# Kernel optimization log

Measured on AMD Instinct MI355X. Metric: run time of the kernel, lower is better.

## Reference

```python
import jax, jax.numpy as jnp
import numpy as np

IN_F = 4096
OUT_F = 11008
GROUP = 128
BATCH = 32
Q_OUT = OUT_F // 2          # two int4 values packed per byte along out dim
N_GROUPS = IN_F // GROUP    # 32 groups


def setup_inputs() -> dict:
    key = jax.random.key(0)
    k1, k2, k3, k4, k5 = jax.random.split(key, 5)
    inp = jax.random.normal(k1, (BATCH, 1, IN_F), dtype=jnp.float32)
    qweight = jax.random.randint(k2, (IN_F, Q_OUT), 0, 256, dtype=jnp.int32)   # packed bytes
    scales = jax.random.uniform(k3, (N_GROUPS, OUT_F), dtype=jnp.float32) * 0.01
    qzeros = jax.random.randint(k4, (N_GROUPS, Q_OUT), 0, 256, dtype=jnp.int32)  # packed bytes
    bias = jax.random.normal(k5, (OUT_F,), dtype=jnp.float32)
    return {"input": inp, "qweight": qweight, "scales": scales, "qzeros": qzeros, "bias": bias}


def _unpack_int4(packed, n_out):
    # packed: [rows, n_out//2] bytes; low nibble -> even out col, high nibble -> odd out col
    low = packed & 0xF
    high = (packed >> 4) & 0xF
    return jnp.stack([low, high], axis=-1).reshape(packed.shape[0], n_out)


def reference(input, qweight, scales, qzeros, bias):
    # GPTQ-style grouped dequant: w[k, n] = (q[k, n] - zero[g(k), n]) * scale[g(k), n]
    q = _unpack_int4(qweight, OUT_F).astype(jnp.float32)   # [K, N]
    z = _unpack_int4(qzeros, OUT_F).astype(jnp.float32)    # [G, N]
    gidx = jnp.arange(IN_F) // GROUP                       # [K] group index per input channel
    w = (q - z[gidx]) * scales[gidx]                       # [K, N] dequantized weight
    # decode GEMV/GEMM: [B, 1, K] x [K, N] -> [B, 1, N], plus bias (mm_bias_int4 path)
    return jnp.einsum('bsk,kn->bsn', input, w) + bias
```

## Files before the change

### kernel.cpp

```cpp
#include <hip/hip_runtime.h>
#include <cstdint>

#define IN_F 4096
#define OUT_F 11008
#define Q_OUT 5504
#define GROUP 128
#define BATCH 32

#define KBS 8
#define GPB 4
#define NCH 8
#define BN 64
#define BST 18
#define DEPTH 4

typedef int   i32x4 __attribute__((ext_vector_type(4)));
typedef float f32x4 __attribute__((ext_vector_type(4)));

__global__ __launch_bounds__(256)
void prep_kernel(const float* __restrict__ x,
                 const float* __restrict__ bias,
                 uint4* __restrict__ xq,
                 int*   __restrict__ Sx,
                 float* __restrict__ delta,
                 float* __restrict__ out)
{
    const int t = threadIdx.x;
    if (blockIdx.x >= 32) {
        const int base = (blockIdx.x - 32) * 4096 + t * 16;
        #pragma unroll
        for (int i = 0; i < 4; ++i)
            *reinterpret_cast<float4*>(out + base + i * 4) =
                *reinterpret_cast<const float4*>(bias + ((base + i * 4) % OUT_F));
        return;
    }
    const int m = blockIdx.x;
    const float* xr = x + (size_t)m * IN_F + t * 16;
    float4 v[4];
    #pragma unroll
    for (int i = 0; i < 4; ++i) v[i] = reinterpret_cast<const float4*>(xr)[i];

    float lm = 0.f;
    #pragma unroll
    for (int i = 0; i < 4; ++i) {
        lm = fmaxf(lm, fmaxf(fmaxf(fabsf(v[i].x), fabsf(v[i].y)),
                             fmaxf(fabsf(v[i].z), fabsf(v[i].w))));
    }
    #pragma unroll
    for (int d = 32; d; d >>= 1) lm = fmaxf(lm, __shfl_xor(lm, d));
    __shared__ float wred[4];
    if ((t & 63) == 0) wred[t >> 6] = lm;
    __syncthreads();
    const float mx  = fmaxf(fmaxf(wred[0], wred[1]), fmaxf(wred[2], wred[3]));
    const float inv = mx > 0.f ? 127.0f / mx : 0.f;

    int q[16];
    #pragma unroll
    for (int i = 0; i < 4; ++i) {
        q[i * 4 + 0] = __float2int_rn(v[i].x * inv);
        q[i * 4 + 1] = __float2int_rn(v[i].y * inv);
        q[i * 4 + 2] = __float2int_rn(v[i].z * inv);
        q[i * 4 + 3] = __float2int_rn(v[i].w * inv);
    }
    uint4 w;
    uint* wp = reinterpret_cast<uint*>(&w);
    #pragma unroll
    for (int i = 0; i < 4; ++i)
        wp[i] = (q[i*4] & 255) | ((q[i*4+1] & 255) << 8) |
                ((q[i*4+2] & 255) << 16) | ((q[i*4+3] & 255) << 24);
    xq[(t >> 2) * 128 + (m >> 4) * 64 + (t & 3) * 16 + (m & 15)] = w;

    int psum = 0;
    #pragma unroll
    for (int i = 0; i < 16; ++i) psum += q[i];
    #pragma unroll
    for (int d = 4; d; d >>= 1) psum += __shfl_down(psum, d, 8);
    if ((t & 7) == 0) Sx[(t >> 3) * 32 + m] = psum;
    if (t == 0) delta[m] = mx * (1.0f / 127.0f);
}

__global__ __launch_bounds__(256, 4)
void int4_gemm_i8(const uint4* __restrict__ xq,
                  const int*   __restrict__ qw,
                  const float* __restrict__ scales,
                  const int*   __restrict__ qz,
                  const int*   __restrict__ Sx,
                  const float* __restrict__ delta,
                  float*       __restrict__ out)
{
    const int tid  = threadIdx.x;
    const int lane = tid & 63;
    const int wid  = tid >> 6;
    const int nb   = blockIdx.x;
    const int kb   = blockIdx.y;
    const int g0   = kb * GPB;
    const int k0b  = g0 * GROUP;

    __shared__ uint4 a_lds[1024];
    __shared__ int   b_lds[2][64 * BST];

    const int cl  = lane & 15;
    const int kg  = lane >> 4;
    const int n   = nb * BN + wid * 16 + cl;
    const int shn = (cl & 1) * 4;

    #pragma unroll
    for (int r = 0; r < 4; ++r) {
        const uint4* gp = xq + (size_t)kb * 1024 + r * 256 + tid;
        __builtin_amdgcn_global_load_lds(
            (const __attribute__((address_space(1))) uint32_t*)gp,
            (__attribute__((address_space(3))) uint32_t*)&a_lds[r * 256 + wid * 64],
            16, 0, 0);
    }

    int   zv[GPB];
    float sv[GPB];
    #pragma unroll
    for (int g = 0; g < GPB; ++g) {
        sv[g] = scales[(size_t)(g0 + g) * OUT_F + n];
        zv[g] = (qz[(size_t)(g0 + g) * Q_OUT + (n >> 1)] >> shn) & 15;
    }

    const int a16 = tid & 15;
    const int rk  = tid >> 4;

    uint2 d[DEPTH][4];
    i32x4 acc_i[2] = {};
    f32x4 accf[2]  = {};
    int4  sx0v = {}, sx1v = {};

    auto LOADB = [&](int c, int set) {
        const int kr = k0b + c * 64 + 4 * rk;
        #pragma unroll
        for (int i = 0; i < 4; ++i)
            d[set][i] = *reinterpret_cast<const uint2*>(
                qw + (size_t)(kr + i) * Q_OUT + nb * 32 + 2 * a16);
    };
    auto WLDS = [&](int buf, int set) {
        #pragma unroll
        for (int j = 0; j < 2; ++j) {
            uint b0 = (j ? d[set][0].y : d[set][0].x) & 255u;
            uint b1 = (j ? d[set][1].y : d[set][1].x) & 255u;
            uint b2 = (j ? d[set][2].y : d[set][2].x) & 255u;
            uint b3 = (j ? d[set][3].y : d[set][3].x) & 255u;
            uint p  = b0 | (b1 << 8) | (b2 << 16) | (b3 << 24);
            const int nloc = 4 * a16 + 2 * j;
            b_lds[buf][(nloc + 0) * BST + rk] = (int)(p & 0x0F0F0F0Fu);
            b_lds[buf][(nloc + 1) * BST + rk] = (int)((p >> 4) & 0x0F0F0F0Fu);
        }
    };

    LOADB(0, 0);
    LOADB(1, 1);
    LOADB(2, 2);
    LOADB(3, 3);
    WLDS(0, 0);
    asm volatile("s_waitcnt vmcnt(0) lgkmcnt(0)" ::: "memory");
    __builtin_amdgcn_s_barrier();
    asm volatile("" ::: "memory");

    #pragma unroll
    for (int c = 0; c < NCH; ++c) {
        const int cur = c & 1;
        const int gl  = c >> 1;
        if (c + DEPTH < NCH) LOADB(c + DEPTH, c & 3);
        if ((c & 1) == 0) {
            sx0v = *reinterpret_cast<const int4*>(Sx + (g0 + gl) * 32 + kg * 4);
            sx1v = *reinterpret_cast<const int4*>(Sx + (g0 + gl) * 32 + 16 + kg * 4);
        }

        const int* bp = &b_lds[cur][(wid * 16 + cl) * BST + 4 * kg];
        int2 qa = *reinterpret_cast<const int2*>(bp);
        int2 qb = *reinterpret_cast<const int2*>(bp + 2);
        i32x4 bv; bv[0] = qa.x; bv[1] = qa.y; bv[2] = qb.x; bv[3] = qb.y;

        uint4 a0 = a_lds[(c * 2 + 0) * 64 + lane];
        uint4 a1 = a_lds[(c * 2 + 1) * 64 + lane];
        acc_i[0] = __builtin_amdgcn_mfma_i32_16x16x64_i8(
            __builtin_bit_cast(i32x4, a0), bv, acc_i[0], 0, 0, 0);
        acc_i[1] = __builtin_amdgcn_mfma_i32_16x16x64_i8(
            __builtin_bit_cast(i32x4, a1), bv, acc_i[1], 0, 0, 0);

        if (c & 1) {
            const int   zz = zv[gl];
            const float ss = sv[gl];
            int sxa[8] = { sx0v.x, sx0v.y, sx0v.z, sx0v.w,
                           sx1v.x, sx1v.y, sx1v.z, sx1v.w };
            #pragma unroll
            for (int f = 0; f < 2; ++f)
                #pragma unroll
                for (int r = 0; r < 4; ++r) {
                    int tt = acc_i[f][r] - zz * sxa[f * 4 + r];
                    accf[f][r] = fmaf(ss, (float)tt, accf[f][r]);
                }
            acc_i[0] = i32x4{0, 0, 0, 0};
            acc_i[1] = i32x4{0, 0, 0, 0};
        }

        if (c + 1 < NCH) {
            WLDS(cur ^ 1, (c + 1) & 3);
            asm volatile("s_waitcnt lgkmcnt(0)" ::: "memory");
            __builtin_amdgcn_s_barrier();
            asm volatile("" ::: "memory");
        }
    }

    float4 dl0 = *reinterpret_cast<const float4*>(delta + kg * 4);
    float4 dl1 = *reinterpret_cast<const float4*>(delta + 16 + kg * 4);
    const float dla[8] = { dl0.x, dl0.y, dl0.z, dl0.w, dl1.x, dl1.y, dl1.z, dl1.w };
    #pragma unroll
    for (int f = 0; f < 2; ++f)
        #pragma unroll
        for (int r = 0; r < 4; ++r) {
            const int m = f * 16 + kg * 4 + r;
            unsafeAtomicAdd(out + (size_t)m * OUT_F + n, dla[f * 4 + r] * accf[f][r]);
        }
}

extern "C" void kernel_launch(void* const* d_in, const int* in_sizes, int n_in,
                              void* d_out, int out_size, void* d_ws, size_t ws_size,
                              hipStream_t stream)
{
    const float* inp    = (const float*)d_in[0];
    const int*   qw     = (const int*)d_in[1];
    const float* scales = (const float*)d_in[2];
    const int*   qz     = (const int*)d_in[3];
    const float* bias   = (const float*)d_in[4];
    float*       out    = (float*)d_out;

    uint4* xq    = (uint4*)d_ws;
    int*   Sx    = (int*)((char*)d_ws + 131072);
    float* delta = (float*)((char*)d_ws + 131072 + 4096);

    prep_kernel<<<118, 256, 0, stream>>>(inp, bias, xq, Sx, delta, out);

    int4_gemm_i8<<<dim3(OUT_F / BN, KBS), 256, 0, stream>>>(
        xq, qw, scales, qz, Sx, delta, out);
}
```

Before: 27.96 us.

## Split K across twice as many blocks and load activations directly to registers

```diff
diff --git a/kernel.cpp b/kernel.cpp
--- a/kernel.cpp
+++ b/kernel.cpp
@@ -7,12 +7,11 @@
 #define GROUP 128
 #define BATCH 32
 
-#define KBS 8
-#define GPB 4
-#define NCH 8
+#define KBS 16
+#define GPB 2
+#define NCH 4
 #define BN 64
 #define BST 18
-#define DEPTH 4
 
 typedef int   i32x4 __attribute__((ext_vector_type(4)));
 typedef float f32x4 __attribute__((ext_vector_type(4)));
@@ -94,25 +93,35 @@
     const int nb   = blockIdx.x;
     const int kb   = blockIdx.y;
     const int g0   = kb * GPB;
-    const int k0b  = g0 * GROUP;
-
-    __shared__ uint4 a_lds[1024];
-    __shared__ int   b_lds[2][64 * BST];
+    const int k0b  = kb * (NCH * 64);
+
+    __shared__ int b_lds[2][64 * BST];
 
     const int cl  = lane & 15;
     const int kg  = lane >> 4;
     const int n   = nb * BN + wid * 16 + cl;
     const int shn = (cl & 1) * 4;
 
-    #pragma unroll
-    for (int r = 0; r < 4; ++r) {
-        const uint4* gp = xq + (size_t)kb * 1024 + r * 256 + tid;
-        __builtin_amdgcn_global_load_lds(
-            (const __attribute__((address_space(1))) uint32_t*)gp,
-            (__attribute__((address_space(3))) uint32_t*)&a_lds[r * 256 + wid * 64],
-            16, 0, 0);
-    }
-
+    const int a16 = tid & 15;
+    const int rk  = tid >> 4;
+
+    uint2 d[NCH][4];
+    uint4 A[NCH][2];
+
+    #pragma unroll
+    for (int c = 0; c < NCH; ++c) {
+        const int kr = k0b + c * 64 + 4 * rk;
+        #pragma unroll
+        for (int i = 0; i < 4; ++i)
+            d[c][i] = *reinterpret_cast<const uint2*>(
+                qw + (size_t)(kr + i) * Q_OUT + nb * 32 + 2 * a16);
+    }
+    #pragma unroll
+    for (int c = 0; c < NCH; ++c) {
+        const uint4* ab = xq + (size_t)(kb * NCH + c) * 128;
+        A[c][0] = ab[lane];
+        A[c][1] = ab[64 + lane];
+    }
     int   zv[GPB];
     float sv[GPB];
     #pragma unroll
@@ -121,21 +130,6 @@
         zv[g] = (qz[(size_t)(g0 + g) * Q_OUT + (n >> 1)] >> shn) & 15;
     }
 
-    const int a16 = tid & 15;
-    const int rk  = tid >> 4;
-
-    uint2 d[DEPTH][4];
-    i32x4 acc_i[2] = {};
-    f32x4 accf[2]  = {};
-    int4  sx0v = {}, sx1v = {};
-
-    auto LOADB = [&](int c, int set) {
-        const int kr = k0b + c * 64 + 4 * rk;
-        #pragma unroll
-        for (int i = 0; i < 4; ++i)
-            d[set][i] = *reinterpret_cast<const uint2*>(
-                qw + (size_t)(kr + i) * Q_OUT + nb * 32 + 2 * a16);
-    };
     auto WLDS = [&](int buf, int set) {
         #pragma unroll
         for (int j = 0; j < 2; ++j) {
@@ -150,12 +144,12 @@
         }
     };
 
-    LOADB(0, 0);
-    LOADB(1, 1);
-    LOADB(2, 2);
-    LOADB(3, 3);
+    i32x4 acc_i[2] = {};
+    f32x4 accf[2]  = {};
+    int4  sx0v = {}, sx1v = {};
+
     WLDS(0, 0);
-    asm volatile("s_waitcnt vmcnt(0) lgkmcnt(0)" ::: "memory");
+    asm volatile("s_waitcnt lgkmcnt(0)" ::: "memory");
     __builtin_amdgcn_s_barrier();
     asm volatile("" ::: "memory");
 
@@ -163,7 +157,6 @@
     for (int c = 0; c < NCH; ++c) {
         const int cur = c & 1;
         const int gl  = c >> 1;
-        if (c + DEPTH < NCH) LOADB(c + DEPTH, c & 3);
         if ((c & 1) == 0) {
             sx0v = *reinterpret_cast<const int4*>(Sx + (g0 + gl) * 32 + kg * 4);
             sx1v = *reinterpret_cast<const int4*>(Sx + (g0 + gl) * 32 + 16 + kg * 4);
@@ -174,12 +167,10 @@
         int2 qb = *reinterpret_cast<const int2*>(bp + 2);
         i32x4 bv; bv[0] = qa.x; bv[1] = qa.y; bv[2] = qb.x; bv[3] = qb.y;
 
-        uint4 a0 = a_lds[(c * 2 + 0) * 64 + lane];
-        uint4 a1 = a_lds[(c * 2 + 1) * 64 + lane];
         acc_i[0] = __builtin_amdgcn_mfma_i32_16x16x64_i8(
-            __builtin_bit_cast(i32x4, a0), bv, acc_i[0], 0, 0, 0);
+            __builtin_bit_cast(i32x4, A[c][0]), bv, acc_i[0], 0, 0, 0);
         acc_i[1] = __builtin_amdgcn_mfma_i32_16x16x64_i8(
-            __builtin_bit_cast(i32x4, a1), bv, acc_i[1], 0, 0, 0);
+            __builtin_bit_cast(i32x4, A[c][1]), bv, acc_i[1], 0, 0, 0);
 
         if (c & 1) {
             const int   zz = zv[gl];
@@ -198,7 +189,7 @@
         }
 
         if (c + 1 < NCH) {
-            WLDS(cur ^ 1, (c + 1) & 3);
+            WLDS(cur ^ 1, c + 1);
             asm volatile("s_waitcnt lgkmcnt(0)" ::: "memory");
             __builtin_amdgcn_s_barrier();
             asm volatile("" ::: "memory");
```

Result: slower. 31.81 us (+13.8%).

## Repack int4 weights into MFMA tile layout and load operands directly to registers

Applied to the files above, without the earlier changes.

```diff
diff --git a/kernel.cpp b/kernel.cpp
--- a/kernel.cpp
+++ b/kernel.cpp
@@ -10,9 +10,7 @@
 #define KBS 8
 #define GPB 4
 #define NCH 8
-#define BN 64
 #define BST 18
-#define DEPTH 4
 
 typedef int   i32x4 __attribute__((ext_vector_type(4)));
 typedef float f32x4 __attribute__((ext_vector_type(4)));
@@ -42,10 +40,9 @@
 
     float lm = 0.f;
     #pragma unroll
-    for (int i = 0; i < 4; ++i) {
+    for (int i = 0; i < 4; ++i)
         lm = fmaxf(lm, fmaxf(fmaxf(fabsf(v[i].x), fabsf(v[i].y)),
                              fmaxf(fabsf(v[i].z), fabsf(v[i].w))));
-    }
     #pragma unroll
     for (int d = 32; d; d >>= 1) lm = fmaxf(lm, __shfl_xor(lm, d));
     __shared__ float wred[4];
@@ -79,9 +76,36 @@
     if (t == 0) delta[m] = mx * (1.0f / 127.0f);
 }
 
+__global__ __launch_bounds__(256)
+void repack_kernel(const int* __restrict__ qw, uint4* __restrict__ qb)
+{
+    const int t    = threadIdx.x;
+    const int lane = t & 63;
+    const int rq   = t >> 6;
+    const int pc   = blockIdx.x * 64 + lane;
+    const int kb   = blockIdx.y;
+    const int W    = pc >> 3;
+    const int p    = pc & 7;
+
+    #pragma unroll 1
+    for (int c = 0; c < 8; ++c) {
+        const int krow = kb * 512 + c * 64 + rq * 16;
+        const int* src = qw + (size_t)krow * Q_OUT + pc;
+        uint b[16];
+        #pragma unroll
+        for (int i = 0; i < 16; ++i) b[i] = (uint)src[(size_t)i * Q_OUT] & 255u;
+        uint4 w;
+        w.x = b[0]  | (b[1]  << 8) | (b[2]  << 16) | (b[3]  << 24);
+        w.y = b[4]  | (b[5]  << 8) | (b[6]  << 16) | (b[7]  << 24);
+        w.z = b[8]  | (b[9]  << 8) | (b[10] << 16) | (b[11] << 24);
+        w.w = b[12] | (b[13] << 8) | (b[14] << 16) | (b[15] << 24);
+        qb[((size_t)(W * 8 + kb) * 8 + c) * 32 + p * 4 + rq] = w;
+    }
+}
+
 __global__ __launch_bounds__(256, 4)
-void int4_gemm_i8(const uint4* __restrict__ xq,
-                  const int*   __restrict__ qw,
+void int4_gemm_qb(const uint4* __restrict__ xq,
+                  const uint4* __restrict__ qb,
                   const float* __restrict__ scales,
                   const int*   __restrict__ qz,
                   const int*   __restrict__ Sx,
@@ -91,27 +115,15 @@
     const int tid  = threadIdx.x;
     const int lane = tid & 63;
     const int wid  = tid >> 6;
-    const int nb   = blockIdx.x;
+    const int W    = blockIdx.x * 4 + wid;
     const int kb   = blockIdx.y;
     const int g0   = kb * GPB;
-    const int k0b  = g0 * GROUP;
-
-    __shared__ uint4 a_lds[1024];
-    __shared__ int   b_lds[2][64 * BST];
 
     const int cl  = lane & 15;
     const int kg  = lane >> 4;
-    const int n   = nb * BN + wid * 16 + cl;
+    const int n   = W * 16 + cl;
+    const int p   = cl >> 1;
     const int shn = (cl & 1) * 4;
-
-    #pragma unroll
-    for (int r = 0; r < 4; ++r) {
-        const uint4* gp = xq + (size_t)kb * 1024 + r * 256 + tid;
-        __builtin_amdgcn_global_load_lds(
-            (const __attribute__((address_space(1))) uint32_t*)gp,
-            (__attribute__((address_space(3))) uint32_t*)&a_lds[r * 256 + wid * 64],
-            16, 0, 0);
-    }
 
     int   zv[GPB];
     float sv[GPB];
@@ -121,65 +133,48 @@
         zv[g] = (qz[(size_t)(g0 + g) * Q_OUT + (n >> 1)] >> shn) & 15;
     }
 
-    const int a16 = tid & 15;
-    const int rk  = tid >> 4;
-
-    uint2 d[DEPTH][4];
+    const size_t btile = ((size_t)(W * 8 + kb) * 8) * 32 + p * 4 + kg;
+    const size_t atile = (size_t)kb * 1024;
+
+    uint4 B[4];
+    uint4 A[4][2];
+    #pragma unroll
+    for (int c = 0; c < 4; ++c) {
+        B[c]    = qb[btile + (size_t)c * 32];
+        A[c][0] = xq[atile + (size_t)c * 128 + lane];
+        A[c][1] = xq[atile + (size_t)c * 128 + 64 + lane];
+    }
+
     i32x4 acc_i[2] = {};
     f32x4 accf[2]  = {};
     int4  sx0v = {}, sx1v = {};
 
-    auto LOADB = [&](int c, int set) {
-        const int kr = k0b + c * 64 + 4 * rk;
-        #pragma unroll
-        for (int i = 0; i < 4; ++i)
-            d[set][i] = *reinterpret_cast<const uint2*>(
-                qw + (size_t)(kr + i) * Q_OUT + nb * 32 + 2 * a16);
-    };
-    auto WLDS = [&](int buf, int set) {
-        #pragma unroll
-        for (int j = 0; j < 2; ++j) {
-            uint b0 = (j ? d[set][0].y : d[set][0].x) & 255u;
-            uint b1 = (j ? d[set][1].y : d[set][1].x) & 255u;
-            uint b2 = (j ? d[set][2].y : d[set][2].x) & 255u;
-            uint b3 = (j ? d[set][3].y : d[set][3].x) & 255u;
-            uint p  = b0 | (b1 << 8) | (b2 << 16) | (b3 << 24);
-            const int nloc = 4 * a16 + 2 * j;
-            b_lds[buf][(nloc + 0) * BST + rk] = (int)(p & 0x0F0F0F0Fu);
-            b_lds[buf][(nloc + 1) * BST + rk] = (int)((p >> 4) & 0x0F0F0F0Fu);
-        }
-    };
-
-    LOADB(0, 0);
-    LOADB(1, 1);
-    LOADB(2, 2);
-    LOADB(3, 3);
-    WLDS(0, 0);
-    asm volatile("s_waitcnt vmcnt(0) lgkmcnt(0)" ::: "memory");
-    __builtin_amdgcn_s_barrier();
-    asm volatile("" ::: "memory");
-
     #pragma unroll
     for (int c = 0; c < NCH; ++c) {
-        const int cur = c & 1;
-        const int gl  = c >> 1;
-        if (c + DEPTH < NCH) LOADB(c + DEPTH, c & 3);
+        const int s  = c & 3;
+        const int gl = c >> 1;
         if ((c & 1) == 0) {
             sx0v = *reinterpret_cast<const int4*>(Sx + (g0 + gl) * 32 + kg * 4);
             sx1v = *reinterpret_cast<const int4*>(Sx + (g0 + gl) * 32 + 16 + kg * 4);
         }
 
-        const int* bp = &b_lds[cur][(wid * 16 + cl) * BST + 4 * kg];
-        int2 qa = *reinterpret_cast<const int2*>(bp);
-        int2 qb = *reinterpret_cast<const int2*>(bp + 2);
-        i32x4 bv; bv[0] = qa.x; bv[1] = qa.y; bv[2] = qb.x; bv[3] = qb.y;
-
-        uint4 a0 = a_lds[(c * 2 + 0) * 64 + lane];
-        uint4 a1 = a_lds[(c * 2 + 1) * 64 + lane];
+        uint4 bq = B[s];
+        i32x4 bv;
+        bv[0] = (int)((bq.x >> shn) & 0x0F0F0F0Fu);
+        bv[1] = (int)((bq.y >> shn) & 0x0F0F0F0Fu);
+        bv[2] = (int)((bq.z >> shn) & 0x0F0F0F0Fu);
+        bv[3] = (int)((bq.w >> shn) & 0x0F0F0F0Fu);
+
         acc_i[0] = __builtin_amdgcn_mfma_i32_16x16x64_i8(
-            __builtin_bit_cast(i32x4, a0), bv, acc_i[0], 0, 0, 0);
+            __builtin_bit_cast(i32x4, A[s][0]), bv, acc_i[0], 0, 0, 0);
         acc_i[1] = __builtin_amdgcn_mfma_i32_16x16x64_i8(
-            __builtin_bit_cast(i32x4, a1), bv, acc_i[1], 0, 0, 0);
+            __builtin_bit_cast(i32x4, A[s][1]), bv, acc_i[1], 0, 0, 0);
+
+        if (c + 4 < NCH) {
+            B[s]    = qb[btile + (size_t)(c + 4) * 32];
+            A[s][0] = xq[atile + (size_t)(c + 4) * 128 + lane];
+            A[s][1] = xq[atile + (size_t)(c + 4) * 128 + 64 + lane];
+        }
 
         if (c & 1) {
             const int   zz = zv[gl];
@@ -196,9 +191,138 @@
             acc_i[0] = i32x4{0, 0, 0, 0};
             acc_i[1] = i32x4{0, 0, 0, 0};
         }
+    }
+
+    float4 dl0 = *reinterpret_cast<const float4*>(delta + kg * 4);
+    float4 dl1 = *reinterpret_cast<const float4*>(delta + 16 + kg * 4);
+    const float dla[8] = { dl0.x, dl0.y, dl0.z, dl0.w, dl1.x, dl1.y, dl1.z, dl1.w };
+    #pragma unroll
+    for (int f = 0; f < 2; ++f)
+        #pragma unroll
+        for (int r = 0; r < 4; ++r) {
+            const int m = f * 16 + kg * 4 + r;
+            unsafeAtomicAdd(out + (size_t)m * OUT_F + n, dla[f * 4 + r] * accf[f][r]);
+        }
+}
+
+__global__ __launch_bounds__(256, 4)
+void int4_gemm_fb(const uint4* __restrict__ xq,
+                  const int*   __restrict__ qw,
+                  const float* __restrict__ scales,
+                  const int*   __restrict__ qz,
+                  const int*   __restrict__ Sx,
+                  const float* __restrict__ delta,
+                  float*       __restrict__ out)
+{
+    const int tid  = threadIdx.x;
+    const int lane = tid & 63;
+    const int wid  = tid >> 6;
+    const int nb   = blockIdx.x;
+    const int kb   = blockIdx.y;
+    const int g0   = kb * GPB;
+    const int k0b  = g0 * GROUP;
+
+    __shared__ uint4 a_lds[1024];
+    __shared__ int   b_lds[2][64 * BST];
+
+    const int cl  = lane & 15;
+    const int kg  = lane >> 4;
+    const int n   = nb * 64 + wid * 16 + cl;
+    const int shn = (cl & 1) * 4;
+
+    #pragma unroll
+    for (int r = 0; r < 4; ++r) {
+        const uint4* gp = xq + (size_t)kb * 1024 + r * 256 + tid;
+        __builtin_amdgcn_global_load_lds(
+            (const __attribute__((address_space(1))) uint32_t*)gp,
+            (__attribute__((address_space(3))) uint32_t*)&a_lds[r * 256 + wid * 64],
+            16, 0, 0);
+    }
+
+    int   zv[GPB];
+    float sv[GPB];
+    #pragma unroll
+    for (int g = 0; g < GPB; ++g) {
+        sv[g] = scales[(size_t)(g0 + g) * OUT_F + n];
+        zv[g] = (qz[(size_t)(g0 + g) * Q_OUT + (n >> 1)] >> shn) & 15;
+    }
+
+    const int a16 = tid & 15;
+    const int rk  = tid >> 4;
+
+    uint2 d[2][4];
+    i32x4 acc_i[2] = {};
+    f32x4 accf[2]  = {};
+    int4  sx0v = {}, sx1v = {};
+
+    auto LOADB = [&](int c, int set) {
+        const int kr = k0b + c * 64 + 4 * rk;
+        #pragma unroll
+        for (int i = 0; i < 4; ++i)
+            d[set][i] = *reinterpret_cast<const uint2*>(
+                qw + (size_t)(kr + i) * Q_OUT + nb * 32 + 2 * a16);
+    };
+    auto WLDS = [&](int buf, int set) {
+        #pragma unroll
+        for (int j = 0; j < 2; ++j) {
+            uint b0 = (j ? d[set][0].y : d[set][0].x) & 255u;
+            uint b1 = (j ? d[set][1].y : d[set][1].x) & 255u;
+            uint b2 = (j ? d[set][2].y : d[set][2].x) & 255u;
+            uint b3 = (j ? d[set][3].y : d[set][3].x) & 255u;
+            uint p  = b0 | (b1 << 8) | (b2 << 16) | (b3 << 24);
+            const int nloc = 4 * a16 + 2 * j;
+            b_lds[buf][(nloc + 0) * BST + rk] = (int)(p & 0x0F0F0F0Fu);
+            b_lds[buf][(nloc + 1) * BST + rk] = (int)((p >> 4) & 0x0F0F0F0Fu);
+        }
+    };
+
+    LOADB(0, 0);
+    LOADB(1, 1);
+    WLDS(0, 0);
+    asm volatile("s_waitcnt vmcnt(0) lgkmcnt(0)" ::: "memory");
+    __builtin_amdgcn_s_barrier();
+    asm volatile("" ::: "memory");
+
+    #pragma unroll
+    for (int c = 0; c < NCH; ++c) {
+        const int cur = c & 1;
+        const int gl  = c >> 1;
+        if (c + 2 < NCH) LOADB(c + 2, cur);
+        if ((c & 1) == 0) {
+            sx0v = *reinterpret_cast<const int4*>(Sx + (g0 + gl) * 32 + kg * 4);
+            sx1v = *reinterpret_cast<const int4*>(Sx + (g0 + gl) * 32 + 16 + kg * 4);
+        }
+
+        const int* bp = &b_lds[cur][(wid * 16 + cl) * BST + 4 * kg];
+        int2 qa = *reinterpret_cast<const int2*>(bp);
+        int2 qb2 = *reinterpret_cast<const int2*>(bp + 2);
+        i32x4 bv; bv[0] = qa.x; bv[1] = qa.y; bv[2] = qb2.x; bv[3] = qb2.y;
+
+        uint4 a0 = a_lds[(c * 2 + 0) * 64 + lane];
+        uint4 a1 = a_lds[(c * 2 + 1) * 64 + lane];
+        acc_i[0] = __builtin_amdgcn_mfma_i32_16x16x64_i8(
+            __builtin_bit_cast(i32x4, a0), bv, acc_i[0], 0, 0, 0);
+        acc_i[1] = __builtin_amdgcn_mfma_i32_16x16x64_i8(
+            __builtin_bit_cast(i32x4, a1), bv, acc_i[1], 0, 0, 0);
+
+        if (c & 1) {
+            const int   zz = zv[gl];
+            const float ss = sv[gl];
+            int sxa[8] = { sx0v.x, sx0v.y, sx0v.z, sx0v.w,
+                           sx1v.x, sx1v.y, sx1v.z, sx1v.w };
+            #pragma unroll
+            for (int f = 0; f < 2; ++f)
+                #pragma unroll
+                for (int r = 0; r < 4; ++r) {
+                    int tt = acc_i[f][r] - zz * sxa[f * 4 + r];
+                    accf[f][r] = fmaf(ss, (float)tt, accf[f][r]);
+                }
+            acc_i[0] = i32x4{0, 0, 0, 0};
+            acc_i[1] = i32x4{0, 0, 0, 0};
+        }
 
         if (c + 1 < NCH) {
-            WLDS(cur ^ 1, (c + 1) & 3);
+            WLDS(cur ^ 1, cur ^ 1);
             asm volatile("s_waitcnt lgkmcnt(0)" ::: "memory");
             __builtin_amdgcn_s_barrier();
             asm volatile("" ::: "memory");
@@ -232,8 +356,18 @@
     int*   Sx    = (int*)((char*)d_ws + 131072);
     float* delta = (float*)((char*)d_ws + 131072 + 4096);
 
+    const size_t QB_OFF   = (size_t)1 << 20;
+    const size_t QB_BYTES = (size_t)688 * 8 * 8 * 512;
+
     prep_kernel<<<118, 256, 0, stream>>>(inp, bias, xq, Sx, delta, out);
 
-    int4_gemm_i8<<<dim3(OUT_F / BN, KBS), 256, 0, stream>>>(
-        xq, qw, scales, qz, Sx, delta, out);
-}
+    if (ws_size >= QB_OFF + QB_BYTES) {
+        uint4* qb = (uint4*)((char*)d_ws + QB_OFF);
+        repack_kernel<<<dim3(Q_OUT / 64, KBS), 256, 0, stream>>>(qw, qb);
+        int4_gemm_qb<<<dim3(688 / 4, KBS), 256, 0, stream>>>(
+            xq, qb, scales, qz, Sx, delta, out);
+    } else {
+        int4_gemm_fb<<<dim3(OUT_F / 64, KBS), 256, 0, stream>>>(
+            xq, qw, scales, qz, Sx, delta, out);
+    }
+}
```

New measurement: 43.88 us. 1.57x slower.
